# Performance work log

Hardware: AMD Instinct MI355X
Metric: run time of the kernel (lower is better)

The kernel has to match this reference:

```python
import jax, jax.numpy as jnp
import numpy as np

WINDOW_SIZE = 8
NUM_HEADS = 16
KAN_GRID = 5
GRID_MIN, GRID_MAX = -2.0, 2.0


def _relative_position_index(ws: int) -> np.ndarray:
    # Same construction as the Keras __init__: pairwise 2D relative coords -> flat index
    coords = np.stack(np.meshgrid(np.arange(ws), np.arange(ws), indexing='ij'))  # [2,ws,ws]
    flat = coords.reshape(2, -1)                                                 # [2,N]
    rel = flat[:, :, None] - flat[:, None, :]                                    # [2,N,N]
    rel = rel.transpose(1, 2, 0)                                                 # [N,N,2]
    rh = (rel[:, :, 0] + ws - 1) * (2 * ws - 1)
    rw = rel[:, :, 1] + ws - 1
    return (rh + rw).astype(np.int32)                                            # [N,N]

_REL_IDX = _relative_position_index(WINDOW_SIZE)


def setup_inputs() -> dict:
    key = jax.random.key(0)
    ks = jax.random.split(key, 8)
    B, N, C = 512, WINDOW_SIZE * WINDOW_SIZE, 512
    G = KAN_GRID
    s = 0.02
    return {
        'x': jax.random.normal(ks[0], (B, N, C), jnp.float32),
        'Wq': jax.random.normal(ks[1], (C, C), jnp.float32) * s,
        'Wk_base': jax.random.normal(ks[2], (C, C), jnp.float32) * s,
        'Wk_spline': jax.random.normal(ks[3], (C * G, C), jnp.float32) * s,
        'Wv': jax.random.normal(ks[4], (C, C), jnp.float32) * s,
        'Wproj': jax.random.normal(ks[5], (C, C), jnp.float32) * s,
        'bproj': jnp.zeros((C,), jnp.float32),
        'bias_table': jax.random.normal(ks[6], ((2 * WINDOW_SIZE - 1) ** 2, NUM_HEADS), jnp.float32) * s,
    }


def _kan_key(x, W_base, W_spline):
    # FastKAN-style KANLinear: base path = swish(x) @ W_base,
    # spline path = Gaussian-RBF basis over each input channel, linearly combined.
    B, N, C = x.shape
    G = KAN_GRID
    grid = jnp.linspace(GRID_MIN, GRID_MAX, G).astype(x.dtype)          # [G]
    h = (GRID_MAX - GRID_MIN) / (G - 1)
    phi = jnp.exp(-(((x[..., None] - grid) / h) ** 2))                  # [B,N,C,G]
    spline = phi.reshape(B, N, C * G) @ W_spline                        # [B,N,C]
    base = jax.nn.swish(x) @ W_base                                     # [B,N,C]
    return base + spline


def reference(x, Wq, Wk_base, Wk_spline, Wv, Wproj, bproj, bias_table):
    B, N, C = x.shape
    H = NUM_HEADS
    hd = C // H
    scale = hd ** -0.5

    def split_heads(t):  # [B,N,C] -> [B,H,N,hd]
        return t.reshape(B, N, H, hd).transpose(0, 2, 1, 3)

    q = split_heads(x @ Wq)
    k = split_heads(_kan_key(x, Wk_base, Wk_spline))
    v = split_heads(x @ Wv)

    scores = jnp.einsum('bhnd,bhmd->bhnm', q, k) * scale                # [B,H,N,N]
    bias = bias_table[_REL_IDX]                                         # [N,N,H]
    scores = scores + bias.transpose(2, 0, 1)[None]                     # + [1,H,N,N]
    # internal padding mask: input already fills the full window, mask is all-ones -> no-op,
    # kept structurally: mask==0 positions would be set to large negative before softmax.
    attn = jax.nn.softmax(scores, axis=-1)
    ctx = jnp.einsum('bhnm,bhmd->bhnd', attn, v)                        # [B,H,N,hd]
    ctx = ctx.transpose(0, 2, 1, 3).reshape(B, N, C)
    return ctx @ Wproj + bproj
```

## Files before the change

kernel.cpp:

```cpp
#include <hip/hip_runtime.h>
#include <hip/hip_bf16.h>

using bf16 = __bf16;
typedef __bf16 bf16x8 __attribute__((ext_vector_type(8)));
typedef __bf16 bf16x4 __attribute__((ext_vector_type(4)));
typedef float  f32x4  __attribute__((ext_vector_type(4)));

__device__ __forceinline__ void gl2lds16(const bf16* g, bf16* l)
{
    __builtin_amdgcn_global_load_lds(
        (const __attribute__((address_space(1))) unsigned int*)g,
        (__attribute__((address_space(3))) unsigned int*)l,
        16, 0, 0);
}

__global__ void prep(const float* __restrict__ x, bf16* __restrict__ xb,
                     bf16* __restrict__ swb, int n)
{
    int base = (blockIdx.x * 256 + threadIdx.x) * 8;
    if (base >= n) return;
    float4 a = *(const float4*)(x + base);
    float4 b = *(const float4*)(x + base + 4);
    float xs[8] = {a.x, a.y, a.z, a.w, b.x, b.y, b.z, b.w};
    bf16x8 xo, so;
#pragma unroll
    for (int t = 0; t < 8; ++t) {
        xo[t] = (bf16)xs[t];
        so[t] = (bf16)(xs[t] / (1.0f + __expf(-xs[t])));
    }
    *(bf16x8*)(xb  + base) = xo;
    *(bf16x8*)(swb + base) = so;
}

__global__ void transpose_k(const float* __restrict__ W, bf16* __restrict__ Wt,
                            int K, int N, int ldT, int total)
{
    int idx = blockIdx.x * 256 + threadIdx.x;
    if (idx >= total) return;
    int k = idx % K;
    int n = idx / K;
    Wt[(size_t)n * ldT + k] = (bf16)W[(size_t)k * N + n];
}

template<int AMODE, bool BIAS, typename CT>
__global__ __launch_bounds__(512, 4)
void gemm_bt(const bf16* __restrict__ A, const float* __restrict__ X,
             const bf16* __restrict__ Bt, CT* __restrict__ C,
             int M, int K, const float* __restrict__ bias)
{
    __shared__ bf16 As0[64 * 32],  As1[64 * 32];
    __shared__ bf16 Bs0[512 * 32], Bs1[512 * 32];

    const int tid  = threadIdx.x;
    const int lane = tid & 63;
    const int wave = tid >> 6;
    const int quad = lane >> 4;
    const int l15  = lane & 15;
    const int m0   = blockIdx.x * 64;

    f32x4 acc[4][4] = {};
    float xr3[3];

    auto stage_b = [&](bf16* Bs, int kt) {
#pragma unroll
        for (int cc = 0; cc < 4; ++cc) {
            const int chunk = cc * 512 + tid;
            const int row   = chunk >> 2;
            const int col8  = (chunk & 3) * 8;
            gl2lds16(Bt + (size_t)row * K + kt + col8, Bs + chunk * 8);
        }
    };
    auto stage_a_copy = [&](bf16* As, int kt) {
        if (tid < 256) {
            const int row  = tid >> 2;
            const int col8 = (tid & 3) * 8;
            const int ld   = (AMODE == 0) ? K : 512;
            gl2lds16(A + (size_t)(m0 + row) * ld + kt + col8, As + tid * 8);
        }
    };
    auto phi_load = [&](int kt) {
        if (tid < 256) {
            const int col8 = (tid & 3) * 8;
            const int ks   = kt + col8 - 512;
            const int c0   = ks / 5;
            const int row  = tid >> 2;
            const float* xr = X + (size_t)(m0 + row) * 512 + c0;
            xr3[0] = xr[0];
            xr3[1] = xr[1];
            xr3[2] = xr[(c0 < 510) ? 2 : 1];
        }
    };
    auto phi_store = [&](bf16* As, int kt) {
        if (tid < 256) {
            const int row  = tid >> 2;
            const int col8 = (tid & 3) * 8;
            const int ks   = kt + col8 - 512;
            const int c0   = ks / 5;
            const int r0   = ks - c0 * 5;
            bf16x8 o;
            float xv = xr3[0], xnext = xr3[1];
            int g = r0;
#pragma unroll
            for (int t = 0; t < 8; ++t) {
                float d = xv - (float)(g - 2);
                o[t] = (bf16)__expf(-d * d);
                if (++g == 5) { g = 0; xv = xnext; xnext = xr3[2]; }
            }
            *(bf16x8*)(As + row * 32 + col8) = o;
        }
    };
    auto compute = [&](const bf16* As, const bf16* Bs) {
        bf16x8 af[4], bfr[4];
#pragma unroll
        for (int i = 0; i < 4; ++i)
            af[i] = *(const bf16x8*)(As + (i * 16 + l15) * 32 + quad * 8);
#pragma unroll
        for (int j = 0; j < 4; ++j)
            bfr[j] = *(const bf16x8*)(Bs + (wave * 64 + j * 16 + l15) * 32 + quad * 8);
#pragma unroll
        for (int i = 0; i < 4; ++i)
#pragma unroll
            for (int j = 0; j < 4; ++j)
                acc[i][j] = __builtin_amdgcn_mfma_f32_16x16x32_bf16(af[i], bfr[j], acc[i][j], 0, 0, 0);
    };

    stage_b(Bs0, 0);
    stage_a_copy(As0, 0);
    __syncthreads();

    bf16 *Ac = As0, *Bc = Bs0, *Aa = As1, *Ba = Bs1;

    const int NT = K >> 5;
    for (int t = 0; t < NT; ++t) {
        const int  kn       = (t + 1) << 5;
        const bool havenext = (t + 1 < NT);
        const bool nextphi  = (AMODE == 2) && (kn >= 512);
        if (havenext) {
            if (nextphi) phi_load(kn);
            stage_b(Ba, kn);
            if (!nextphi) stage_a_copy(Aa, kn);
        }
        compute(Ac, Bc);
        if (havenext && nextphi) phi_store(Aa, kn);
        __syncthreads();
        bf16* s;
        s = Ac; Ac = Aa; Aa = s;
        s = Bc; Bc = Ba; Ba = s;
    }

#pragma unroll
    for (int i = 0; i < 4; ++i) {
#pragma unroll
        for (int j = 0; j < 4; ++j) {
            const int col = wave * 64 + j * 16 + l15;
            const float bv = BIAS ? bias[col] : 0.0f;
#pragma unroll
            for (int r = 0; r < 4; ++r) {
                const int row = m0 + i * 16 + quad * 4 + r;
                C[(size_t)row * 512 + col] = (CT)(acc[i][j][r] + bv);
            }
        }
    }
}

__global__ __launch_bounds__(256)
void attn_mfma(const bf16* __restrict__ q, const bf16* __restrict__ k,
               const bf16* __restrict__ v, const float* __restrict__ bias_table,
               bf16* __restrict__ ctx)
{
    constexpr int LQ = 40;
    constexpr int LV = 72;
    __shared__ bf16 qs[64 * LQ];
    __shared__ bf16 ks[64 * LQ];
    __shared__ bf16 vsT[32 * LV];
    __shared__ bf16 Pl[4][16 * LV];
    __shared__ float bl[225];

    const int bid  = blockIdx.x;
    const int b    = bid >> 4;
    const int h    = bid & 15;
    const int tid  = threadIdx.x;
    const int lane = tid & 63;
    const int w    = tid >> 6;
    const int quad = lane >> 4;
    const int l15  = lane & 15;

    const int n  = tid >> 2;
    const int d0 = (tid & 3) * 8;
    const size_t gbase = ((size_t)(b * 64 + n)) * 512 + h * 32 + d0;
    {
        bf16x8 rq = *(const bf16x8*)(q + gbase);
        bf16x8 rk = *(const bf16x8*)(k + gbase);
        bf16x8 rv = *(const bf16x8*)(v + gbase);
        *(bf16x8*)(qs + n * LQ + d0) = rq;
        *(bf16x8*)(ks + n * LQ + d0) = rk;
#pragma unroll
        for (int t = 0; t < 8; ++t) vsT[(d0 + t) * LV + n] = rv[t];
    }
    if (tid < 225) bl[tid] = bias_table[tid * 16 + h];
    __syncthreads();

    f32x4 sacc[4] = {};
    {
        bf16x8 aq = *(const bf16x8*)(qs + (w * 16 + l15) * LQ + quad * 8);
#pragma unroll
        for (int j = 0; j < 4; ++j) {
            bf16x8 bk = *(const bf16x8*)(ks + (j * 16 + l15) * LQ + quad * 8);
            sacc[j] = __builtin_amdgcn_mfma_f32_16x16x32_bf16(aq, bk, sacc[j], 0, 0, 0);
        }
    }

    bf16* Pw = Pl[w];
    float inv[4];
    {
        const float scale = 0.17677669529663687f;
#pragma unroll
        for (int r = 0; r < 4; ++r) {
            const int row = w * 16 + quad * 4 + r;
            const int rh = row >> 3, rw = row & 7;
            float pv[4];
            float mx = -1e30f;
#pragma unroll
            for (int j = 0; j < 4; ++j) {
                const int c   = j * 16 + l15;
                const int idx = (rh - (c >> 3) + 7) * 15 + (rw - (c & 7) + 7);
                float s = sacc[j][r] * scale + bl[idx];
                pv[j] = s;
                mx = fmaxf(mx, s);
            }
            mx = fmaxf(mx, __shfl_xor(mx, 1, 64));
            mx = fmaxf(mx, __shfl_xor(mx, 2, 64));
            mx = fmaxf(mx, __shfl_xor(mx, 4, 64));
            mx = fmaxf(mx, __shfl_xor(mx, 8, 64));
            float sum = 0.0f;
#pragma unroll
            for (int j = 0; j < 4; ++j) {
                float e = __expf(pv[j] - mx);
                pv[j] = e;
                sum += e;
            }
            sum += __shfl_xor(sum, 1, 64);
            sum += __shfl_xor(sum, 2, 64);
            sum += __shfl_xor(sum, 4, 64);
            sum += __shfl_xor(sum, 8, 64);
            inv[r] = 1.0f / sum;
#pragma unroll
            for (int j = 0; j < 4; ++j)
                Pw[(quad * 4 + r) * LV + j * 16 + l15] = (bf16)pv[j];
        }
    }

    f32x4 oacc[2] = {};
#pragma unroll
    for (int mc = 0; mc < 2; ++mc) {
        bf16x8 ap = *(const bf16x8*)(Pw + l15 * LV + mc * 32 + quad * 8);
#pragma unroll
        for (int dt = 0; dt < 2; ++dt) {
            bf16x8 bv = *(const bf16x8*)(vsT + (dt * 16 + l15) * LV + mc * 32 + quad * 8);
            oacc[dt] = __builtin_amdgcn_mfma_f32_16x16x32_bf16(ap, bv, oacc[dt], 0, 0, 0);
        }
    }

#pragma unroll
    for (int dt = 0; dt < 2; ++dt)
#pragma unroll
        for (int r = 0; r < 4; ++r)
            qs[(w * 16 + quad * 4 + r) * LQ + dt * 16 + l15] = (bf16)(oacc[dt][r] * inv[r]);

    bf16x8 ov = *(const bf16x8*)(qs + n * LQ + d0);
    *(bf16x8*)(ctx + gbase) = ov;
}

extern "C" void kernel_launch(void* const* d_in, const int* in_sizes, int n_in,
                              void* d_out, int out_size, void* d_ws, size_t ws_size,
                              hipStream_t stream)
{
    const float* x       = (const float*)d_in[0];
    const float* Wq      = (const float*)d_in[1];
    const float* Wk_base = (const float*)d_in[2];
    const float* Wk_spl  = (const float*)d_in[3];
    const float* Wv      = (const float*)d_in[4];
    const float* Wproj   = (const float*)d_in[5];
    const float* bproj   = (const float*)d_in[6];
    const float* btab    = (const float*)d_in[7];

    bf16* ws  = (bf16*)d_ws;
    bf16* wqT = ws;
    bf16* wvT = ws + 262144;
    bf16* wpT = ws + 524288;
    bf16* wkT = ws + 786432;
    bf16* xb  = ws + 2359296;
    bf16* q   = ws + 19136512;
    bf16* kk  = ws + 35913728;
    bf16* swb = (bf16*)d_out;
    bf16* vv  = (bf16*)d_out + 16777216;
    bf16* ctx = q;

    prep<<<8192, 256, 0, stream>>>(x, xb, swb, 16777216);

    transpose_k<<<1024, 256, 0, stream>>>(Wq,      wqT,       512,  512, 512,  262144);
    transpose_k<<<1024, 256, 0, stream>>>(Wv,      wvT,       512,  512, 512,  262144);
    transpose_k<<<1024, 256, 0, stream>>>(Wproj,   wpT,       512,  512, 512,  262144);
    transpose_k<<<1024, 256, 0, stream>>>(Wk_base, wkT,       512,  512, 3072, 262144);
    transpose_k<<<5120, 256, 0, stream>>>(Wk_spl,  wkT + 512, 2560, 512, 3072, 1310720);

    gemm_bt<0, false, bf16><<<512, 512, 0, stream>>>(xb,  nullptr, wqT, q,  32768, 512,  nullptr);
    gemm_bt<2, false, bf16><<<512, 512, 0, stream>>>(swb, x,       wkT, kk, 32768, 3072, nullptr);
    gemm_bt<0, false, bf16><<<512, 512, 0, stream>>>(xb,  nullptr, wvT, vv, 32768, 512,  nullptr);

    attn_mfma<<<8192, 256, 0, stream>>>(q, kk, vv, btab, ctx);

    gemm_bt<0, true, float><<<512, 512, 0, stream>>>(ctx, nullptr, wpT, (float*)d_out, 32768, 512, bproj);
}
```

Before: 421.7 us.

## Split GEMM N into 256-wide tiles, swizzle blocks, and tile weight transposes

Each GEMM block now computes a 64x256 output tile with 256 threads instead of a 64x512 tile with 512 threads. The grid doubles to 1024 blocks and block IDs are remapped across groups of 8 so neighbouring blocks share A or B rows. All threads now take part in A staging and phi generation, so there is no longer an idle half-block during the KAN basis computation. The weight-transpose kernels are rewritten to use a padded 32x32 LDS tile, giving coalesced reads and writes. In exchange, A tiles are loaded twice (once per N half), and for the spline GEMM the phi basis is recomputed twice.

New measurement: 426.0 us. About the same (+1.0%).

```diff
diff --git a/kernel.cpp b/kernel.cpp
--- a/kernel.cpp
+++ b/kernel.cpp
@@ -33,30 +33,41 @@
 }
 
 __global__ void transpose_k(const float* __restrict__ W, bf16* __restrict__ Wt,
-                            int K, int N, int ldT, int total)
-{
-    int idx = blockIdx.x * 256 + threadIdx.x;
-    if (idx >= total) return;
-    int k = idx % K;
-    int n = idx / K;
-    Wt[(size_t)n * ldT + k] = (bf16)W[(size_t)k * N + n];
+                            int K, int N, int ldT)
+{
+    __shared__ float t[32][33];
+    const int k0 = blockIdx.x * 32;
+    const int n0 = blockIdx.y * 32;
+    const int lx = threadIdx.x & 31;
+    const int ly = threadIdx.x >> 5;
+#pragma unroll
+    for (int r = 0; r < 32; r += 8)
+        t[ly + r][lx] = W[(size_t)(k0 + ly + r) * N + n0 + lx];
+    __syncthreads();
+#pragma unroll
+    for (int r = 0; r < 32; r += 8)
+        Wt[(size_t)(n0 + ly + r) * ldT + k0 + lx] = (bf16)t[lx][ly + r];
 }
 
 template<int AMODE, bool BIAS, typename CT>
-__global__ __launch_bounds__(512, 4)
+__global__ __launch_bounds__(256, 4)
 void gemm_bt(const bf16* __restrict__ A, const float* __restrict__ X,
              const bf16* __restrict__ Bt, CT* __restrict__ C,
              int M, int K, const float* __restrict__ bias)
 {
     __shared__ bf16 As0[64 * 32],  As1[64 * 32];
-    __shared__ bf16 Bs0[512 * 32], Bs1[512 * 32];
+    __shared__ bf16 Bs0[256 * 32], Bs1[256 * 32];
+
+    const int nwg = gridDim.x;
+    const int bid = ((int)blockIdx.x & 7) * (nwg >> 3) + ((int)blockIdx.x >> 3);
 
     const int tid  = threadIdx.x;
     const int lane = tid & 63;
     const int wave = tid >> 6;
     const int quad = lane >> 4;
     const int l15  = lane & 15;
-    const int m0   = blockIdx.x * 64;
+    const int m0   = (bid >> 1) * 64;
+    const int n0   = (bid & 1) * 256;
 
     f32x4 acc[4][4] = {};
     float xr3[3];
@@ -64,50 +75,44 @@
     auto stage_b = [&](bf16* Bs, int kt) {
 #pragma unroll
         for (int cc = 0; cc < 4; ++cc) {
-            const int chunk = cc * 512 + tid;
+            const int chunk = cc * 256 + tid;
             const int row   = chunk >> 2;
             const int col8  = (chunk & 3) * 8;
-            gl2lds16(Bt + (size_t)row * K + kt + col8, Bs + chunk * 8);
+            gl2lds16(Bt + (size_t)(n0 + row) * K + kt + col8, Bs + chunk * 8);
         }
     };
     auto stage_a_copy = [&](bf16* As, int kt) {
-        if (tid < 256) {
-            const int row  = tid >> 2;
-            const int col8 = (tid & 3) * 8;
-            const int ld   = (AMODE == 0) ? K : 512;
-            gl2lds16(A + (size_t)(m0 + row) * ld + kt + col8, As + tid * 8);
-        }
+        const int row  = tid >> 2;
+        const int col8 = (tid & 3) * 8;
+        const int ld   = (AMODE == 0) ? K : 512;
+        gl2lds16(A + (size_t)(m0 + row) * ld + kt + col8, As + tid * 8);
     };
     auto phi_load = [&](int kt) {
-        if (tid < 256) {
-            const int col8 = (tid & 3) * 8;
-            const int ks   = kt + col8 - 512;
-            const int c0   = ks / 5;
-            const int row  = tid >> 2;
-            const float* xr = X + (size_t)(m0 + row) * 512 + c0;
-            xr3[0] = xr[0];
-            xr3[1] = xr[1];
-            xr3[2] = xr[(c0 < 510) ? 2 : 1];
-        }
+        const int col8 = (tid & 3) * 8;
+        const int ks   = kt + col8 - 512;
+        const int c0   = ks / 5;
+        const int row  = tid >> 2;
+        const float* xr = X + (size_t)(m0 + row) * 512 + c0;
+        xr3[0] = xr[0];
+        xr3[1] = xr[1];
+        xr3[2] = xr[(c0 < 510) ? 2 : 1];
     };
     auto phi_store = [&](bf16* As, int kt) {
-        if (tid < 256) {
-            const int row  = tid >> 2;
-            const int col8 = (tid & 3) * 8;
-            const int ks   = kt + col8 - 512;
-            const int c0   = ks / 5;
-            const int r0   = ks - c0 * 5;
-            bf16x8 o;
-            float xv = xr3[0], xnext = xr3[1];
-            int g = r0;
-#pragma unroll
-            for (int t = 0; t < 8; ++t) {
-                float d = xv - (float)(g - 2);
-                o[t] = (bf16)__expf(-d * d);
-                if (++g == 5) { g = 0; xv = xnext; xnext = xr3[2]; }
-            }
-            *(bf16x8*)(As + row * 32 + col8) = o;
-        }
+        const int row  = tid >> 2;
+        const int col8 = (tid & 3) * 8;
+        const int ks   = kt + col8 - 512;
+        const int c0   = ks / 5;
+        const int r0   = ks - c0 * 5;
+        bf16x8 o;
+        float xv = xr3[0], xnext = xr3[1];
+        int g = r0;
+#pragma unroll
+        for (int t = 0; t < 8; ++t) {
+            float d = xv - (float)(g - 2);
+            o[t] = (bf16)__expf(-d * d);
+            if (++g == 5) { g = 0; xv = xnext; xnext = xr3[2]; }
+        }
+        *(bf16x8*)(As + row * 32 + col8) = o;
     };
     auto compute = [&](const bf16* As, const bf16* Bs) {
         bf16x8 af[4], bfr[4];
@@ -152,7 +157,7 @@
     for (int i = 0; i < 4; ++i) {
 #pragma unroll
         for (int j = 0; j < 4; ++j) {
-            const int col = wave * 64 + j * 16 + l15;
+            const int col = n0 + wave * 64 + j * 16 + l15;
             const float bv = BIAS ? bias[col] : 0.0f;
 #pragma unroll
             for (int r = 0; r < 4; ++r) {
@@ -298,17 +303,17 @@
 
     prep<<<8192, 256, 0, stream>>>(x, xb, swb, 16777216);
 
-    transpose_k<<<1024, 256, 0, stream>>>(Wq,      wqT,       512,  512, 512,  262144);
-    transpose_k<<<1024, 256, 0, stream>>>(Wv,      wvT,       512,  512, 512,  262144);
-    transpose_k<<<1024, 256, 0, stream>>>(Wproj,   wpT,       512,  512, 512,  262144);
-    transpose_k<<<1024, 256, 0, stream>>>(Wk_base, wkT,       512,  512, 3072, 262144);
-    transpose_k<<<5120, 256, 0, stream>>>(Wk_spl,  wkT + 512, 2560, 512, 3072, 1310720);
-
-    gemm_bt<0, false, bf16><<<512, 512, 0, stream>>>(xb,  nullptr, wqT, q,  32768, 512,  nullptr);
-    gemm_bt<2, false, bf16><<<512, 512, 0, stream>>>(swb, x,       wkT, kk, 32768, 3072, nullptr);
-    gemm_bt<0, false, bf16><<<512, 512, 0, stream>>>(xb,  nullptr, wvT, vv, 32768, 512,  nullptr);
+    transpose_k<<<dim3(16, 16), 256, 0, stream>>>(Wq,      wqT,       512,  512, 512);
+    transpose_k<<<dim3(16, 16), 256, 0, stream>>>(Wv,      wvT,       512,  512, 512);
+    transpose_k<<<dim3(16, 16), 256, 0, stream>>>(Wproj,   wpT,       512,  512, 512);
+    transpose_k<<<dim3(16, 16), 256, 0, stream>>>(Wk_base, wkT,       512,  512, 3072);
+    transpose_k<<<dim3(80, 16), 256, 0, stream>>>(Wk_spl,  wkT + 512, 2560, 512, 3072);
+
+    gemm_bt<0, false, bf16><<<1024, 256, 0, stream>>>(xb,  nullptr, wqT, q,  32768, 512,  nullptr);
+    gemm_bt<2, false, bf16><<<1024, 256, 0, stream>>>(swb, x,       wkT, kk, 32768, 3072, nullptr);
+    gemm_bt<0, false, bf16><<<1024, 256, 0, stream>>>(xb,  nullptr, wvT, vv, 32768, 512,  nullptr);
 
     attn_mfma<<<8192, 256, 0, stream>>>(q, kk, vv, btab, ctx);
 
-    gemm_bt<0, true, float><<<512, 512, 0, stream>>>(ctx, nullptr, wpT, (float*)d_out, 32768, 512, bproj);
-}
+    gemm_bt<0, true, float><<<1024, 256, 0, stream>>>(ctx, nullptr, wpT, (float*)d_out, 32768, 512, bproj);
+}
```
